# Optimization experiments

Hardware: AMD Instinct MI355X
Metric: run time of the kernel (lower is better)

The kernel has to match this reference:

```python
import jax, jax.numpy as jnp
import numpy as np

# Production shapes from the module docstring: cs (B,90,512), cs_p (B,90,256,256), mask (B,256,256)
B, H, LP, W, L = 16, 90, 512, 256, 256
K = 384  # number of valid (non-NaN) columns in cs == number of positive mask pixels per item


def setup_inputs() -> dict:
    key = jax.random.key(0)
    k1, k2, k3 = jax.random.split(key, 3)
    cs = jax.random.normal(k1, (B, H, LP), dtype=jnp.float32)
    # NaN padding after the first K columns (same pattern in every row, as the
    # original's reshape([height, -1]) requires equal valid counts per row)
    cs = jnp.where(jnp.arange(LP) < K, cs, jnp.nan)
    cs_p = jax.random.normal(k2, (B, H, W, L), dtype=jnp.float32)
    # exactly K positive overpass pixels per item, at random flat positions
    perm = jax.vmap(lambda k: jax.random.permutation(k, W * L))(jax.random.split(k3, B))
    mask = jnp.zeros((B, W * L), dtype=jnp.int32)
    mask = mask.at[jnp.arange(B)[:, None], perm[:, :K]].set(1)
    return {"cs": cs, "cs_p": cs_p, "overpass_mask": mask.reshape(B, W, L)}


def _per_item_mse(cs_i, cs_p_i, mask_i):
    # cs_i: (H, LP) with NaN padding; valid columns identical across rows, so
    # torch's cs_i[~isnan(cs_i)].reshape(H, -1) == gather of the K valid columns
    # in ascending column order (stable argsort of the NaN flag, False first).
    cols = jnp.argsort(jnp.isnan(cs_i[0]), stable=True)[:K]            # (K,)
    cs_sel = cs_i[:, cols]                                             # (H, K)
    # torch's cs_p_i[mask.expand(H,-1,-1)].reshape(H, -1): per height-row,
    # masked pixels in row-major (w, l) order -> flat-index gather.
    pos = jnp.argsort(mask_i.reshape(-1) <= 0, stable=True)[:K]        # (K,)
    cs_p_sel = cs_p_i.reshape(cs_p_i.shape[0], -1)[:, pos]             # (H, K)
    return jnp.mean((cs_sel - cs_p_sel) ** 2)


def reference(cs, cs_p, overpass_mask):
    # per-item mean MSE, then mean over batch (matches torch.stack(...).mean())
    return jnp.mean(jax.vmap(_per_item_mse)(cs, cs_p, overpass_mask))
```

## Files before the change

### kernel.cpp

```cpp
#include <hip/hip_runtime.h>

#define B_   16
#define H_   90
#define LP_  512
#define WL_  65536
#define K_   384
#define BHK  (B_ * H_ * K_)

__global__ void zero_kernel(float* __restrict__ out) {
    if (threadIdx.x == 0) out[0] = 0.0f;
}

__global__ __launch_bounds__(1024) void pos_kernel(const int* __restrict__ mask,
                                                   int* __restrict__ pos) {
    const int b = blockIdx.x;
    const int t = threadIdx.x;
    const int SEG = WL_ / 1024;
    const int* m = mask + (size_t)b * WL_;
    const int base = t * SEG;

    int cnt = 0;
    const int4* m4 = (const int4*)(m + base);
    #pragma unroll
    for (int i = 0; i < SEG / 4; ++i) {
        int4 v = m4[i];
        cnt += (v.x != 0) + (v.y != 0) + (v.z != 0) + (v.w != 0);
    }

    __shared__ int s[1024];
    s[t] = cnt;
    __syncthreads();
    for (int off = 1; off < 1024; off <<= 1) {
        int v = (t >= off) ? s[t - off] : 0;
        __syncthreads();
        s[t] += v;
        __syncthreads();
    }
    const int excl = s[t] - cnt;

    int* p = pos + b * K_;
    int w = excl;
    for (int i = 0; i < SEG && w < K_; ++i) {
        if (m[base + i] != 0) {
            p[w] = base + i;
            ++w;
        }
    }
}

__global__ __launch_bounds__(256) void mse_kernel(const float* __restrict__ cs,
                                                  const float* __restrict__ csp,
                                                  const int* __restrict__ pos,
                                                  float* __restrict__ out) {
    const int idx = blockIdx.x * 256 + threadIdx.x;
    float v = 0.0f;
    if (idx < BHK) {
        const int k  = idx % K_;
        const int bh = idx / K_;
        const int b  = bh / H_;
        const float a = cs[(size_t)bh * LP_ + k];
        const int   p = pos[b * K_ + k];
        const float c = csp[(size_t)bh * WL_ + p];
        const float d = a - c;
        v = d * d;
    }

    #pragma unroll
    for (int off = 32; off > 0; off >>= 1) v += __shfl_down(v, off, 64);

    __shared__ float s[4];
    const int lane = threadIdx.x & 63;
    const int wid  = threadIdx.x >> 6;
    if (lane == 0) s[wid] = v;
    __syncthreads();
    if (threadIdx.x == 0) {
        const float sum = s[0] + s[1] + s[2] + s[3];
        atomicAdd(out, sum * (1.0f / (float)BHK));
    }
}

extern "C" void kernel_launch(void* const* d_in, const int* in_sizes, int n_in,
                              void* d_out, int out_size, void* d_ws, size_t ws_size,
                              hipStream_t stream) {
    const float* cs   = (const float*)d_in[0];
    const float* csp  = (const float*)d_in[1];
    const int*   mask = (const int*)d_in[2];
    float* out = (float*)d_out;
    int*   pos = (int*)d_ws;

    zero_kernel<<<1, 64, 0, stream>>>(out);
    pos_kernel<<<B_, 1024, 0, stream>>>(mask, pos);
    mse_kernel<<<(BHK + 255) / 256, 256, 0, stream>>>(cs, csp, pos, out);
}
```

Measured before the change: 493.1 us.

## Split mask compaction into parallel count, scan, scatter kernels

Replaces the 16-block per-item compaction (each thread serially scanning 64 mask entries, plus a 1024-wide shared-memory scan) with a three-kernel pipeline: per-chunk counts across 1024 blocks, a single-block wave-level scan of chunk counts, and a parallel scatter using wave shuffles. The MSE kernel is reshaped to one block per (b,h) row with 384 threads, removing div/mod index math. The zero initialisation is folded into the count kernel. This adds an extra kernel launch in exchange for much wider parallelism in the previously serial position-finding step. The scan relies on each wave's 64 chunk counts matching one batch item, which holds because each item has exactly 64 chunks.

```diff
diff --git a/kernel.cpp b/kernel.cpp
--- a/kernel.cpp
+++ b/kernel.cpp
@@ -1,80 +1,97 @@
 #include <hip/hip_runtime.h>
 
-#define B_   16
-#define H_   90
-#define LP_  512
-#define WL_  65536
-#define K_   384
-#define BHK  (B_ * H_ * K_)
+#define B_     16
+#define H_     90
+#define LP_    512
+#define WL_    65536
+#define K_     384
+#define BHK    (B_ * H_ * K_)
+#define CHUNK  1024
+#define NCHUNK (WL_ / CHUNK)
+#define NBLK   (B_ * NCHUNK)
 
-__global__ void zero_kernel(float* __restrict__ out) {
-    if (threadIdx.x == 0) out[0] = 0.0f;
+__global__ __launch_bounds__(256) void count_kernel(const int* __restrict__ mask,
+                                                    int* __restrict__ cnt,
+                                                    float* __restrict__ out) {
+    if (blockIdx.x == 0 && threadIdx.x == 0) out[0] = 0.0f;
+    const int4 v = ((const int4*)(mask + (size_t)blockIdx.x * CHUNK))[threadIdx.x];
+    int c = (v.x != 0) + (v.y != 0) + (v.z != 0) + (v.w != 0);
+    #pragma unroll
+    for (int off = 32; off > 0; off >>= 1) c += __shfl_down(c, off, 64);
+    __shared__ int s[4];
+    const int lane = threadIdx.x & 63, wid = threadIdx.x >> 6;
+    if (lane == 0) s[wid] = c;
+    __syncthreads();
+    if (threadIdx.x == 0) cnt[blockIdx.x] = s[0] + s[1] + s[2] + s[3];
 }
 
-__global__ __launch_bounds__(1024) void pos_kernel(const int* __restrict__ mask,
-                                                   int* __restrict__ pos) {
-    const int b = blockIdx.x;
+__global__ __launch_bounds__(1024) void scan_kernel(const int* __restrict__ cnt,
+                                                    int* __restrict__ offs) {
     const int t = threadIdx.x;
-    const int SEG = WL_ / 1024;
-    const int* m = mask + (size_t)b * WL_;
-    const int base = t * SEG;
-
-    int cnt = 0;
-    const int4* m4 = (const int4*)(m + base);
+    const int lane = t & 63;
+    const int c = cnt[t];
+    int incl = c;
     #pragma unroll
-    for (int i = 0; i < SEG / 4; ++i) {
-        int4 v = m4[i];
-        cnt += (v.x != 0) + (v.y != 0) + (v.z != 0) + (v.w != 0);
+    for (int d = 1; d < 64; d <<= 1) {
+        const int x = __shfl_up(incl, d, 64);
+        if (lane >= d) incl += x;
     }
-
-    __shared__ int s[1024];
-    s[t] = cnt;
-    __syncthreads();
-    for (int off = 1; off < 1024; off <<= 1) {
-        int v = (t >= off) ? s[t - off] : 0;
-        __syncthreads();
-        s[t] += v;
-        __syncthreads();
-    }
-    const int excl = s[t] - cnt;
-
-    int* p = pos + b * K_;
-    int w = excl;
-    for (int i = 0; i < SEG && w < K_; ++i) {
-        if (m[base + i] != 0) {
-            p[w] = base + i;
-            ++w;
-        }
-    }
+    offs[t] = incl - c;
 }
 
-__global__ __launch_bounds__(256) void mse_kernel(const float* __restrict__ cs,
+__global__ __launch_bounds__(256) void scatter_kernel(const int* __restrict__ mask,
+                                                      const int* __restrict__ offs,
+                                                      int* __restrict__ pos) {
+    const int blk = blockIdx.x;
+    const int b = blk >> 6;
+    const int t = threadIdx.x;
+    const int4 v = ((const int4*)(mask + (size_t)blk * CHUNK))[t];
+    const int f0 = v.x != 0, f1 = v.y != 0, f2 = v.z != 0, f3 = v.w != 0;
+    const int c = f0 + f1 + f2 + f3;
+
+    const int lane = t & 63, wid = t >> 6;
+    int incl = c;
+    #pragma unroll
+    for (int d = 1; d < 64; d <<= 1) {
+        const int x = __shfl_up(incl, d, 64);
+        if (lane >= d) incl += x;
+    }
+    __shared__ int ws[4];
+    if (lane == 63) ws[wid] = incl;
+    __syncthreads();
+    int wbase = 0;
+    for (int wi = 0; wi < wid; ++wi) wbase += ws[wi];
+    const int excl = wbase + incl - c;
+
+    const int gbase = (blk & 63) * CHUNK + t * 4;
+    int w = offs[blk] + excl;
+    int* __restrict__ p = pos + b * K_;
+    if (f0) p[w++] = gbase + 0;
+    if (f1) p[w++] = gbase + 1;
+    if (f2) p[w++] = gbase + 2;
+    if (f3) p[w]   = gbase + 3;
+}
+
+__global__ __launch_bounds__(384) void mse_kernel(const float* __restrict__ cs,
                                                   const float* __restrict__ csp,
                                                   const int* __restrict__ pos,
                                                   float* __restrict__ out) {
-    const int idx = blockIdx.x * 256 + threadIdx.x;
-    float v = 0.0f;
-    if (idx < BHK) {
-        const int k  = idx % K_;
-        const int bh = idx / K_;
-        const int b  = bh / H_;
-        const float a = cs[(size_t)bh * LP_ + k];
-        const int   p = pos[b * K_ + k];
-        const float c = csp[(size_t)bh * WL_ + p];
-        const float d = a - c;
-        v = d * d;
-    }
-
+    const int bh = blockIdx.x;
+    const int b  = bh / H_;
+    const int k  = threadIdx.x;
+    const float a = cs[(size_t)bh * LP_ + k];
+    const int   p = pos[b * K_ + k];
+    const float cpv = csp[(size_t)bh * WL_ + p];
+    const float d = a - cpv;
+    float v = d * d;
     #pragma unroll
     for (int off = 32; off > 0; off >>= 1) v += __shfl_down(v, off, 64);
-
-    __shared__ float s[4];
-    const int lane = threadIdx.x & 63;
-    const int wid  = threadIdx.x >> 6;
+    __shared__ float s[6];
+    const int lane = k & 63, wid = k >> 6;
     if (lane == 0) s[wid] = v;
     __syncthreads();
-    if (threadIdx.x == 0) {
-        const float sum = s[0] + s[1] + s[2] + s[3];
+    if (k == 0) {
+        const float sum = s[0] + s[1] + s[2] + s[3] + s[4] + s[5];
         atomicAdd(out, sum * (1.0f / (float)BHK));
     }
 }
@@ -86,9 +103,13 @@
     const float* csp  = (const float*)d_in[1];
     const int*   mask = (const int*)d_in[2];
     float* out = (float*)d_out;
-    int*   pos = (int*)d_ws;
 
-    zero_kernel<<<1, 64, 0, stream>>>(out);
-    pos_kernel<<<B_, 1024, 0, stream>>>(mask, pos);
-    mse_kernel<<<(BHK + 255) / 256, 256, 0, stream>>>(cs, csp, pos, out);
+    int* pos  = (int*)d_ws;
+    int* cnt  = pos + B_ * K_;
+    int* offs = cnt + NBLK;
+
+    count_kernel  <<<NBLK, 256, 0, stream>>>(mask, cnt, out);
+    scan_kernel   <<<1, 1024, 0, stream>>>(cnt, offs);
+    scatter_kernel<<<NBLK, 256, 0, stream>>>(mask, offs, pos);
+    mse_kernel    <<<B_ * H_, 384, 0, stream>>>(cs, csp, pos, out);
 }
```

Result: faster. 441.4 us (-10.5%).
